# Kernel tuning notes

Measured on AMD Instinct MI355X. Metric: run time of the kernel, lower is better.

The kernel has to match this reference:

```python
import jax, jax.numpy as jnp
import numpy as np

B, C, N = 8, 512, 2048
C8 = C // 8


def setup_inputs() -> dict:
    key = jax.random.key(0)
    ks = jax.random.split(key, 8)
    s = 1.0 / np.sqrt(C)
    return {
        "x": jax.random.normal(ks[0], (B, C, N, 1, 1), jnp.float32),
        "y": jax.random.normal(ks[1], (B, C, N, 1, 1), jnp.float32),
        "Wq": jax.random.normal(ks[2], (C8, C), jnp.float32) * s,
        "bq": jax.random.normal(ks[3], (C8,), jnp.float32) * s,
        "Wk": jax.random.normal(ks[4], (C8, C), jnp.float32) * s,
        "bk": jax.random.normal(ks[5], (C8,), jnp.float32) * s,
        "Wv": jax.random.normal(ks[6], (C, C), jnp.float32) * s,
        "bv": jax.random.normal(ks[7], (C,), jnp.float32) * s,
        "gamma": jnp.zeros((1,), jnp.float32),
    }


def reference(x, y, Wq, bq, Wk, bk, Wv, bv, gamma):
    xs = x[..., 0, 0]  # [B, C, N]
    ys = y[..., 0, 0]  # [B, C, N]
    # 1x1 Conv1d == channel-wise linear
    q = jnp.einsum('oc,bcn->bon', Wq, ys) + bq[None, :, None]  # [B, C8, N]
    k = jnp.einsum('oc,bcn->bon', Wk, xs) + bk[None, :, None]  # [B, C8, N]
    v = jnp.einsum('oc,bcn->bon', Wv, ys) + bv[None, :, None]  # [B, C, N]
    energy = jnp.einsum('bon,bom->bnm', q, k)  # [B, Ny, Nx], unscaled
    attention = jax.nn.softmax(energy, axis=-1)
    # out[b,c,n] = sum_m v[b,c,m] * attention[b,n,m]
    out = jnp.einsum('bcm,bnm->bcn', v, attention)
    out = gamma * out + xs
    return out[..., None, None], attention
```

## Files before the change

### kernel.cpp

```cpp
#include <hip/hip_runtime.h>

#define B_ 8
#define C_ 512
#define N_ 2048
#define C8_ 64

typedef short s16x8 __attribute__((ext_vector_type(8)));
typedef float f32x4 __attribute__((ext_vector_type(4)));

__device__ __forceinline__ ushort bf16_rne(float f) {
    unsigned u = __float_as_uint(f);
    u += 0x7FFFu + ((u >> 16) & 1u);
    return (ushort)(u >> 16);
}
__device__ __forceinline__ float bf16_to_f(ushort h) {
    return __uint_as_float((unsigned)h << 16);
}

__global__ __launch_bounds__(256) void wsplit_kernel(
    const float* __restrict__ Wq, const float* __restrict__ Wk,
    ushort* __restrict__ wqhi, ushort* __restrict__ wqlo,
    ushort* __restrict__ wkhi, ushort* __restrict__ wklo)
{
    int idx = blockIdx.x * 256 + threadIdx.x;
    if (idx >= 2 * C8_ * C_) return;
    bool isq = idx < C8_ * C_;
    int i = isq ? idx : idx - C8_ * C_;
    float f = isq ? Wq[i] : Wk[i];
    ushort h = bf16_rne(f);
    ushort l = bf16_rne(f - bf16_to_f(h));
    if (isq) { wqhi[i] = h; wqlo[i] = l; }
    else     { wkhi[i] = h; wklo[i] = l; }
}

__global__ __launch_bounds__(128) void qk_mfma_kernel(
    const ushort* __restrict__ wqhi, const ushort* __restrict__ wqlo,
    const float* __restrict__ bq,  const float* __restrict__ ysrc,
    const ushort* __restrict__ wkhi, const ushort* __restrict__ wklo,
    const float* __restrict__ bk,  const float* __restrict__ xsrc,
    ushort* __restrict__ qhi, ushort* __restrict__ qlo,
    ushort* __restrict__ khi, ushort* __restrict__ klo)
{
    const int bid = blockIdx.x;
    const int id  = bid & 511;
    const bool isq = bid < 512;
    const ushort* __restrict__ whi  = isq ? wqhi : wkhi;
    const ushort* __restrict__ wlo  = isq ? wqlo : wklo;
    const float*  __restrict__ bias = isq ? bq : bk;
    const float*  __restrict__ src  = isq ? ysrc : xsrc;
    ushort* __restrict__ hi = isq ? qhi : khi;
    ushort* __restrict__ lo = isq ? qlo : klo;

    const int b  = id & 7;
    const int n0 = (id >> 3) * 32;
    const int w  = threadIdx.x >> 6;
    const int l  = threadIdx.x & 63;
    const int lc = l & 15;
    const int lq = l >> 4;
    const int nb = n0 + 16 * w;

    const float* ycol = src + ((unsigned)b * C_ * N_ + nb + lc);

    f32x4 acc[4];
    #pragma unroll
    for (int ot = 0; ot < 4; ++ot) acc[ot] = (f32x4){0.f, 0.f, 0.f, 0.f};

    #pragma unroll 4
    for (int ks = 0; ks < 16; ++ks) {
        const int c0 = ks * 32 + 8 * lq;
        float f[8];
        #pragma unroll
        for (int j = 0; j < 8; ++j)
            f[j] = ycol[(unsigned)(c0 + j) * N_];
        ushort ah[8], al[8];
        #pragma unroll
        for (int j = 0; j < 8; ++j) {
            ah[j] = bf16_rne(f[j]);
            al[j] = bf16_rne(f[j] - bf16_to_f(ah[j]));
        }
        s16x8 ahi, alo;
        #pragma unroll
        for (int j = 0; j < 8; ++j) { ahi[j] = (short)ah[j]; alo[j] = (short)al[j]; }

        #pragma unroll
        for (int ot = 0; ot < 4; ++ot) {
            const unsigned boff = (unsigned)(ot * 16 + lc) * C_ + ks * 32 + 8 * lq;
            s16x8 bhi = *(const s16x8*)(whi + boff);
            s16x8 blo = *(const s16x8*)(wlo + boff);
            f32x4 c = acc[ot];
            c = __builtin_amdgcn_mfma_f32_16x16x32_bf16(ahi, bhi, c, 0, 0, 0);
            c = __builtin_amdgcn_mfma_f32_16x16x32_bf16(ahi, blo, c, 0, 0, 0);
            c = __builtin_amdgcn_mfma_f32_16x16x32_bf16(alo, bhi, c, 0, 0, 0);
            acc[ot] = c;
        }
    }

    #pragma unroll
    for (int ot = 0; ot < 4; ++ot) {
        const int o = ot * 16 + lc;
        const float bs = bias[o];
        #pragma unroll
        for (int i = 0; i < 4; ++i) {
            float v = acc[ot][i] + bs;
            ushort h = bf16_rne(v);
            ushort s = bf16_rne(v - bf16_to_f(h));
            unsigned addr = ((unsigned)b * N_ + nb + lq * 4 + i) * C8_ + o;
            hi[addr] = h;
            lo[addr] = s;
        }
    }
}

__global__ __launch_bounds__(512, 4) void attn_kernel(
    const ushort* __restrict__ qhi, const ushort* __restrict__ qlo,
    const ushort* __restrict__ khi, const ushort* __restrict__ klo,
    float* __restrict__ att,
    const float* __restrict__ x, const float* __restrict__ gamma,
    float* __restrict__ out)
{
    const int b  = blockIdx.x & 7;
    const int n0 = (blockIdx.x >> 3) * 16;
    const int t  = threadIdx.x;
    const int w  = t >> 6;
    const int l  = t & 63;
    const int lc = l & 15;
    const int lq = l >> 4;

    const unsigned abase = ((unsigned)b * N_ + n0 + lc) * C8_ + 8 * lq;
    const s16x8* qhp = (const s16x8*)(qhi + abase);
    const s16x8* qlp = (const s16x8*)(qlo + abase);
    s16x8 ah0 = qhp[0], ah1 = qhp[4];
    s16x8 al0 = qlp[0], al1 = qlp[4];

    const unsigned bbase = ((unsigned)b * N_ + w * 256 + lc) * C8_ + 8 * lq;

    f32x4 acc[16];
    #pragma unroll
    for (int i = 0; i < 16; ++i) acc[i] = (f32x4){0.f, 0.f, 0.f, 0.f};

    #pragma unroll
    for (int ti = 0; ti < 16; ++ti) {
        const s16x8* bh = (const s16x8*)(khi + bbase + (unsigned)ti * 16 * C8_);
        const s16x8* bl = (const s16x8*)(klo + bbase + (unsigned)ti * 16 * C8_);
        s16x8 bh0 = bh[0], bh1 = bh[4];
        s16x8 bl0 = bl[0], bl1 = bl[4];
        f32x4 c = acc[ti];
        c = __builtin_amdgcn_mfma_f32_16x16x32_bf16(ah0, bh0, c, 0, 0, 0);
        c = __builtin_amdgcn_mfma_f32_16x16x32_bf16(ah1, bh1, c, 0, 0, 0);
        c = __builtin_amdgcn_mfma_f32_16x16x32_bf16(ah0, bl0, c, 0, 0, 0);
        c = __builtin_amdgcn_mfma_f32_16x16x32_bf16(ah1, bl1, c, 0, 0, 0);
        c = __builtin_amdgcn_mfma_f32_16x16x32_bf16(al0, bh0, c, 0, 0, 0);
        c = __builtin_amdgcn_mfma_f32_16x16x32_bf16(al1, bh1, c, 0, 0, 0);
        acc[ti] = c;
    }

    #pragma unroll
    for (int ti = 0; ti < 16; ++ti)
        #pragma unroll
        for (int i = 0; i < 4; ++i)
            acc[ti][i] = __expf(acc[ti][i]);

    __shared__ float redsum[16][8];
    float ssum[4];
    #pragma unroll
    for (int i = 0; i < 4; ++i) {
        float s = 0.f;
        #pragma unroll
        for (int ti = 0; ti < 16; ++ti) s += acc[ti][i];
        #pragma unroll
        for (int off = 1; off < 16; off <<= 1)
            s += __shfl_xor(s, off, 64);
        ssum[i] = s;
    }
    if (lc == 0) {
        #pragma unroll
        for (int i = 0; i < 4; ++i) redsum[lq * 4 + i][w] = ssum[i];
    }
    __syncthreads();
    #pragma unroll
    for (int i = 0; i < 4; ++i) {
        float s = redsum[lq * 4 + i][0];
        #pragma unroll
        for (int ww = 1; ww < 8; ++ww) s += redsum[lq * 4 + i][ww];
        float inv = 1.0f / s;
        float* rowp = att + ((unsigned)b * N_ + n0 + lq * 4 + i) * N_ + w * 256 + lc;
        #pragma unroll
        for (int ti = 0; ti < 16; ++ti)
            rowp[ti * 16] = acc[ti][i] * inv;
    }

    if (gamma[0] == 0.0f) {
        #pragma unroll
        for (int p = 0; p < 4; ++p) {
            const int c = p * 128 + (t >> 2);
            const int j = t & 3;
            const unsigned off = ((unsigned)b * C_ + c) * N_ + n0 + 4 * j;
            *(float4*)(out + off) = *(const float4*)(x + off);
        }
    }
}

__global__ __launch_bounds__(256) void v_kernel(
    const float* __restrict__ Wv, const float* __restrict__ bv,
    const float* __restrict__ y, const float* __restrict__ gamma,
    float* __restrict__ v)
{
    if (gamma[0] == 0.0f) return;
    const size_t total = (size_t)B_ * C_ * N_;
    for (size_t idx = (size_t)blockIdx.x * 256 + threadIdx.x; idx < total;
         idx += (size_t)gridDim.x * 256) {
        int n = (int)(idx % N_);
        int o = (int)((idx / N_) % C_);
        int b = (int)(idx / ((size_t)N_ * C_));
        float s = bv[o];
        for (int c = 0; c < C_; ++c)
            s += Wv[o * C_ + c] * y[((size_t)b * C_ + c) * N_ + n];
        v[idx] = s;
    }
}

__global__ __launch_bounds__(256) void out_kernel(
    const float* __restrict__ x, const float* __restrict__ gamma,
    const float* __restrict__ v, const float* __restrict__ att,
    float* __restrict__ out)
{
    const float g = gamma[0];
    if (g == 0.0f) return;
    const size_t nf4 = (size_t)B_ * C_ * N_ / 4;
    const float4* x4 = (const float4*)x;
    float4* o4 = (float4*)out;
    for (size_t i = (size_t)blockIdx.x * blockDim.x + threadIdx.x; i < nf4;
         i += (size_t)gridDim.x * blockDim.x) {
        float4 xv = x4[i];
        size_t base = i * 4;
        int n = (int)(base % N_);
        int cch = (int)((base / N_) % C_);
        int b = (int)(base / ((size_t)N_ * C_));
        const float* vp = v + ((size_t)b * C_ + cch) * N_;
        const float* a0 = att + ((size_t)b * N_ + n) * N_;
        float s0 = 0.f, s1 = 0.f, s2 = 0.f, s3 = 0.f;
        for (int m = 0; m < N_; ++m) {
            float vv = vp[m];
            s0 += vv * a0[m];
            s1 += vv * a0[(size_t)N_ + m];
            s2 += vv * a0[2 * (size_t)N_ + m];
            s3 += vv * a0[3 * (size_t)N_ + m];
        }
        o4[i] = make_float4(g * s0 + xv.x, g * s1 + xv.y, g * s2 + xv.z, g * s3 + xv.w);
    }
}

extern "C" void kernel_launch(void* const* d_in, const int* in_sizes, int n_in,
                              void* d_out, int out_size, void* d_ws, size_t ws_size,
                              hipStream_t stream)
{
    const float* x     = (const float*)d_in[0];
    const float* y     = (const float*)d_in[1];
    const float* Wq    = (const float*)d_in[2];
    const float* bq    = (const float*)d_in[3];
    const float* Wk    = (const float*)d_in[4];
    const float* bk    = (const float*)d_in[5];
    const float* Wv    = (const float*)d_in[6];
    const float* bv    = (const float*)d_in[7];
    const float* gamma = (const float*)d_in[8];

    float* out = (float*)d_out;
    float* att = (float*)d_out + (size_t)B_ * C_ * N_;

    char* ws = (char*)d_ws;
    ushort* wqhi = (ushort*)(ws);
    ushort* wqlo = (ushort*)(ws + (64u << 10));
    ushort* wkhi = (ushort*)(ws + (128u << 10));
    ushort* wklo = (ushort*)(ws + (192u << 10));
    ushort* qhi  = (ushort*)(ws + (1u << 20));
    ushort* qlo  = (ushort*)(ws + (3u << 20));
    ushort* khi  = (ushort*)(ws + (5u << 20));
    ushort* klo  = (ushort*)(ws + (7u << 20));
    float*  vbuf = (float*) (ws + (9u << 20));

    wsplit_kernel<<<(2 * C8_ * C_ + 255) / 256, 256, 0, stream>>>(
        Wq, Wk, wqhi, wqlo, wkhi, wklo);

    qk_mfma_kernel<<<1024, 128, 0, stream>>>(
        wqhi, wqlo, bq, y, wkhi, wklo, bk, x, qhi, qlo, khi, klo);

    attn_kernel<<<1024, 512, 0, stream>>>(qhi, qlo, khi, klo, att, x, gamma, out);

    v_kernel<<<1024, 256, 0, stream>>>(Wv, bv, y, gamma, vbuf);
    out_kernel<<<2048, 256, 0, stream>>>(x, gamma, vbuf, att, out);
}
```

Before: 318.4 us.

## Stage attention rows through shared memory for coalesced float4 stores

Attention output rows are staged in a 64KB shared buffer, eight rows at a time, then written out as contiguous float4 stores instead of strided scalar stores. The residual copy of x into out is moved to the start of the kernel so it can overlap with the MFMA work. The occupancy hint drops from 4 to 2 blocks per SM to fit the larger shared allocation. This adds barriers and LDS traffic in exchange for fully coalesced global writes of the large attention matrix.

```diff
diff --git a/kernel.cpp b/kernel.cpp
--- a/kernel.cpp
+++ b/kernel.cpp
@@ -111,7 +111,7 @@
     }
 }
 
-__global__ __launch_bounds__(512, 4) void attn_kernel(
+__global__ __launch_bounds__(512, 2) void attn_kernel(
     const ushort* __restrict__ qhi, const ushort* __restrict__ qlo,
     const ushort* __restrict__ khi, const ushort* __restrict__ klo,
     float* __restrict__ att,
@@ -125,6 +125,16 @@
     const int l  = t & 63;
     const int lc = l & 15;
     const int lq = l >> 4;
+
+    if (gamma[0] == 0.0f) {
+        #pragma unroll
+        for (int p = 0; p < 4; ++p) {
+            const int c = p * 128 + (t >> 2);
+            const int j = t & 3;
+            const unsigned off = ((unsigned)b * C_ + c) * N_ + n0 + 4 * j;
+            *(float4*)(out + off) = *(const float4*)(x + off);
+        }
+    }
 
     const unsigned abase = ((unsigned)b * N_ + n0 + lc) * C8_ + 8 * lq;
     const s16x8* qhp = (const s16x8*)(qhi + abase);
@@ -160,7 +170,8 @@
         for (int i = 0; i < 4; ++i)
             acc[ti][i] = __expf(acc[ti][i]);
 
-    __shared__ float redsum[16][8];
+    __shared__ float smem[8 * 2048];
+
     float ssum[4];
     #pragma unroll
     for (int i = 0; i < 4; ++i) {
@@ -174,29 +185,39 @@
     }
     if (lc == 0) {
         #pragma unroll
-        for (int i = 0; i < 4; ++i) redsum[lq * 4 + i][w] = ssum[i];
+        for (int i = 0; i < 4; ++i) smem[(lq * 4 + i) * 8 + w] = ssum[i];
     }
     __syncthreads();
+    float inv[4];
     #pragma unroll
     for (int i = 0; i < 4; ++i) {
-        float s = redsum[lq * 4 + i][0];
-        #pragma unroll
-        for (int ww = 1; ww < 8; ++ww) s += redsum[lq * 4 + i][ww];
-        float inv = 1.0f / s;
-        float* rowp = att + ((unsigned)b * N_ + n0 + lq * 4 + i) * N_ + w * 256 + lc;
-        #pragma unroll
-        for (int ti = 0; ti < 16; ++ti)
-            rowp[ti * 16] = acc[ti][i] * inv;
-    }
-
-    if (gamma[0] == 0.0f) {
-        #pragma unroll
-        for (int p = 0; p < 4; ++p) {
-            const int c = p * 128 + (t >> 2);
-            const int j = t & 3;
-            const unsigned off = ((unsigned)b * C_ + c) * N_ + n0 + 4 * j;
-            *(float4*)(out + off) = *(const float4*)(x + off);
-        }
+        float s = smem[(lq * 4 + i) * 8 + 0];
+        #pragma unroll
+        for (int ww = 1; ww < 8; ++ww) s += smem[(lq * 4 + i) * 8 + ww];
+        inv[i] = 1.0f / s;
+    }
+    __syncthreads();
+
+    #pragma unroll
+    for (int h = 0; h < 2; ++h) {
+        if ((lq >> 1) == h) {
+            const int rbase = (lq & 1) * 4;
+            #pragma unroll
+            for (int ti = 0; ti < 16; ++ti)
+                #pragma unroll
+                for (int i = 0; i < 4; ++i)
+                    smem[(rbase + i) * 2048 + w * 256 + ti * 16 + lc] =
+                        acc[ti][i] * inv[i];
+        }
+        __syncthreads();
+        const int r = t >> 6;
+        const int f = t & 63;
+        float4* dst = (float4*)(att + ((unsigned)b * N_ + n0 + 8 * h + r) * N_);
+        const float4* srcp = (const float4*)(smem + r * 2048);
+        #pragma unroll
+        for (int j = 0; j < 8; ++j)
+            dst[f + 64 * j] = srcp[f + 64 * j];
+        if (h == 0) __syncthreads();
     }
 }
 
```

Result: slower. 332.0 us (+4.3%).

## Split attention into row-sum pass and recompute-and-store pass

Applied to the files above, without the earlier changes.

The single attention kernel, which kept all 16 tiles of exponentiated energies in registers until the row sums were known, is split in two. The first kernel computes only the softmax denominators and writes their reciprocals to a workspace buffer. The second recomputes QK^T with MFMA, applies exp and the reciprocal, and streams each tile out with nontemporal stores. The x-to-out copy moves to the start of the first kernel and also uses nontemporal stores. This is meant to cut register pressure and let the attention writes overlap with compute, at the cost of doing the QK^T MFMA work twice plus an extra launch.

```diff
diff --git a/kernel.cpp b/kernel.cpp
--- a/kernel.cpp
+++ b/kernel.cpp
@@ -111,10 +111,10 @@
     }
 }
 
-__global__ __launch_bounds__(512, 4) void attn_kernel(
+__global__ __launch_bounds__(512, 4) void attn_sum_kernel(
     const ushort* __restrict__ qhi, const ushort* __restrict__ qlo,
     const ushort* __restrict__ khi, const ushort* __restrict__ klo,
-    float* __restrict__ att,
+    float* __restrict__ inv_sums,
     const float* __restrict__ x, const float* __restrict__ gamma,
     float* __restrict__ out)
 {
@@ -125,6 +125,17 @@
     const int l  = t & 63;
     const int lc = l & 15;
     const int lq = l >> 4;
+
+    if (gamma[0] == 0.0f) {
+        #pragma unroll
+        for (int p = 0; p < 4; ++p) {
+            const int c = p * 128 + (t >> 2);
+            const int j = t & 3;
+            const unsigned off = ((unsigned)b * C_ + c) * N_ + n0 + 4 * j;
+            f32x4 xv = *(const f32x4*)(x + off);
+            __builtin_nontemporal_store(xv, (f32x4*)(out + off));
+        }
+    }
 
     const unsigned abase = ((unsigned)b * N_ + n0 + lc) * C8_ + 8 * lq;
     const s16x8* qhp = (const s16x8*)(qhi + abase);
@@ -177,25 +188,59 @@
         for (int i = 0; i < 4; ++i) redsum[lq * 4 + i][w] = ssum[i];
     }
     __syncthreads();
-    #pragma unroll
-    for (int i = 0; i < 4; ++i) {
-        float s = redsum[lq * 4 + i][0];
-        #pragma unroll
-        for (int ww = 1; ww < 8; ++ww) s += redsum[lq * 4 + i][ww];
-        float inv = 1.0f / s;
-        float* rowp = att + ((unsigned)b * N_ + n0 + lq * 4 + i) * N_ + w * 256 + lc;
-        #pragma unroll
-        for (int ti = 0; ti < 16; ++ti)
-            rowp[ti * 16] = acc[ti][i] * inv;
-    }
-
-    if (gamma[0] == 0.0f) {
-        #pragma unroll
-        for (int p = 0; p < 4; ++p) {
-            const int c = p * 128 + (t >> 2);
-            const int j = t & 3;
-            const unsigned off = ((unsigned)b * C_ + c) * N_ + n0 + 4 * j;
-            *(float4*)(out + off) = *(const float4*)(x + off);
+    if (t < 16) {
+        float s = redsum[t][0];
+        #pragma unroll
+        for (int ww = 1; ww < 8; ++ww) s += redsum[t][ww];
+        inv_sums[(unsigned)b * N_ + n0 + t] = 1.0f / s;
+    }
+}
+
+__global__ __launch_bounds__(512, 4) void attn_store_kernel(
+    const ushort* __restrict__ qhi, const ushort* __restrict__ qlo,
+    const ushort* __restrict__ khi, const ushort* __restrict__ klo,
+    const float* __restrict__ inv_sums, float* __restrict__ att)
+{
+    const int b  = blockIdx.x & 7;
+    const int n0 = (blockIdx.x >> 3) * 16;
+    const int t  = threadIdx.x;
+    const int w  = t >> 6;
+    const int l  = t & 63;
+    const int lc = l & 15;
+    const int lq = l >> 4;
+
+    const unsigned abase = ((unsigned)b * N_ + n0 + lc) * C8_ + 8 * lq;
+    const s16x8* qhp = (const s16x8*)(qhi + abase);
+    const s16x8* qlp = (const s16x8*)(qlo + abase);
+    s16x8 ah0 = qhp[0], ah1 = qhp[4];
+    s16x8 al0 = qlp[0], al1 = qlp[4];
+
+    float inv[4];
+    #pragma unroll
+    for (int i = 0; i < 4; ++i)
+        inv[i] = inv_sums[(unsigned)b * N_ + n0 + lq * 4 + i];
+
+    const unsigned bbase = ((unsigned)b * N_ + w * 256 + lc) * C8_ + 8 * lq;
+
+    #pragma unroll
+    for (int ti = 0; ti < 16; ++ti) {
+        const s16x8* bh = (const s16x8*)(khi + bbase + (unsigned)ti * 16 * C8_);
+        const s16x8* bl = (const s16x8*)(klo + bbase + (unsigned)ti * 16 * C8_);
+        s16x8 bh0 = bh[0], bh1 = bh[4];
+        s16x8 bl0 = bl[0], bl1 = bl[4];
+        f32x4 c = (f32x4){0.f, 0.f, 0.f, 0.f};
+        c = __builtin_amdgcn_mfma_f32_16x16x32_bf16(ah0, bh0, c, 0, 0, 0);
+        c = __builtin_amdgcn_mfma_f32_16x16x32_bf16(ah1, bh1, c, 0, 0, 0);
+        c = __builtin_amdgcn_mfma_f32_16x16x32_bf16(ah0, bl0, c, 0, 0, 0);
+        c = __builtin_amdgcn_mfma_f32_16x16x32_bf16(ah1, bl1, c, 0, 0, 0);
+        c = __builtin_amdgcn_mfma_f32_16x16x32_bf16(al0, bh0, c, 0, 0, 0);
+        c = __builtin_amdgcn_mfma_f32_16x16x32_bf16(al1, bh1, c, 0, 0, 0);
+        const unsigned col = (unsigned)w * 256 + ti * 16 + lc;
+        #pragma unroll
+        for (int i = 0; i < 4; ++i) {
+            float v = __expf(c[i]) * inv[i];
+            __builtin_nontemporal_store(
+                v, att + ((unsigned)b * N_ + n0 + lq * 4 + i) * N_ + col);
         }
     }
 }
@@ -276,7 +321,8 @@
     ushort* qlo  = (ushort*)(ws + (3u << 20));
     ushort* khi  = (ushort*)(ws + (5u << 20));
     ushort* klo  = (ushort*)(ws + (7u << 20));
-    float*  vbuf = (float*) (ws + (9u << 20));
+    float*  invs = (float*) (ws + (9u << 20));
+    float*  vbuf = (float*) (ws + (10u << 20));
 
     wsplit_kernel<<<(2 * C8_ * C_ + 255) / 256, 256, 0, stream>>>(
         Wq, Wk, wqhi, wqlo, wkhi, wklo);
@@ -284,7 +330,11 @@
     qk_mfma_kernel<<<1024, 128, 0, stream>>>(
         wqhi, wqlo, bq, y, wkhi, wklo, bk, x, qhi, qlo, khi, klo);
 
-    attn_kernel<<<1024, 512, 0, stream>>>(qhi, qlo, khi, klo, att, x, gamma, out);
+    attn_sum_kernel<<<1024, 512, 0, stream>>>(
+        qhi, qlo, khi, klo, invs, x, gamma, out);
+
+    attn_store_kernel<<<1024, 512, 0, stream>>>(
+        qhi, qlo, khi, klo, invs, att);
 
     v_kernel<<<1024, 256, 0, stream>>>(Wv, bv, y, gamma, vbuf);
     out_kernel<<<2048, 256, 0, stream>>>(x, gamma, vbuf, att, out);
```

New measurement: 366.0 us. 15.0% more time.
